# Performance work log

Hardware: AMD Instinct MI355X
Metric: run time of the kernel (lower is better)

Reference implementation:

```python
import jax, jax.numpy as jnp
import numpy as np

B, S, D, H = 1, 256, 128, 4
HD = D // H          # 32
EPS = 1e-5
SCALE = 1.0 / float(np.sqrt(HD))


def setup_inputs() -> dict:
    key = jax.random.key(0)
    ks = jax.random.split(key, 6)
    pair = jax.random.normal(ks[0], (B, S, S, D), dtype=jnp.float32)
    ln_w = jnp.ones((D,), dtype=jnp.float32)
    wq = jax.random.normal(ks[1], (D, D), dtype=jnp.float32) * 0.05
    wk = jax.random.normal(ks[2], (D, D), dtype=jnp.float32) * 0.05
    wv = jax.random.normal(ks[3], (D, D), dtype=jnp.float32) * 0.05
    wo = jax.random.normal(ks[4], (D, D), dtype=jnp.float32) * 0.05
    return {"pair": pair, "ln_w": ln_w, "wq": wq, "wk": wk, "wv": wv, "wo": wo}


def reference(pair, ln_w, wq, wk, wv, wo):
    b, s, _, d = pair.shape
    h, hd = H, HD
    # LayerNorm (weight only, no bias) over last dim
    mu = jnp.mean(pair, axis=-1, keepdims=True)
    var = jnp.mean((pair - mu) ** 2, axis=-1, keepdims=True)
    xn = (pair - mu) * jax.lax.rsqrt(var + EPS) * ln_w
    # starting=True: no transpose of the pair axes
    q = (xn @ wq.T).reshape(b, s, s, h, hd)
    k = (xn @ wk.T).reshape(b, s, s, h, hd)
    v = (xn @ wv.T).reshape(b, s, s, h, hd)
    # attention over the second seq axis (j), independent per row i
    scores = jnp.einsum("biqhd,bikhd->bihqk", q, k) * SCALE  # [b,i,h,q,k]
    p = jax.nn.softmax(scores, axis=-1)
    out = jnp.einsum("bihqk,bikhd->biqhd", p, v).reshape(b, s, s, d)
    return out @ wo.T
```

## Files before the change

### kernel.cpp

```cpp
#include <hip/hip_runtime.h>
#include <hip/hip_bf16.h>
#include <math.h>

#define S 256
#define D 128
#define H 4
#define HD 32
#define NT (S * S)

constexpr float EPS = 1e-5f;
constexpr float EXPC = 0.17677669529663687f * 1.44269504088896f;

typedef short bf16x8 __attribute__((ext_vector_type(8)));
typedef float floatx4 __attribute__((ext_vector_type(4)));

union BfBits { __hip_bfloat16 b; unsigned short u; };
__device__ inline unsigned short f2bf_bits(float f) {
  BfBits t;
  t.b = __float2bfloat16(f);
  return t.u;
}
__device__ inline short f2bf_s(float f) { return (short)f2bf_bits(f); }
__device__ inline float bfbits2f(unsigned short u) {
  union { float f; unsigned int i; } t;
  t.i = ((unsigned int)u) << 16;
  return t.f;
}
__device__ inline void split_bf(float x, unsigned short& hi, unsigned short& lo) {
  hi = f2bf_bits(x);
  lo = f2bf_bits(x - bfbits2f(hi));
}

__global__ __launch_bounds__(256) void wsplit_kernel(
    const float* __restrict__ wq, const float* __restrict__ wk,
    const float* __restrict__ wv, const float* __restrict__ wo,
    unsigned short* __restrict__ whi, unsigned short* __restrict__ wlo) {
  int idx = blockIdx.x * 256 + threadIdx.x;
  const float* srcs[4] = {wq, wk, wv, wo};
#pragma unroll
  for (int m = 0; m < 4; m++) {
    unsigned short hi, lo;
    split_bf(srcs[m][idx], hi, lo);
    whi[m * 16384 + idx] = hi;
    wlo[m * 16384 + idx] = lo;
  }
}

#define XPAD 8
__global__ __launch_bounds__(256, 4) void qkv_ln_mfma_kernel(
    const float* __restrict__ pair, const float* __restrict__ ln_w,
    const unsigned short* __restrict__ Whi,
    const unsigned short* __restrict__ Wlo, unsigned short* __restrict__ Qb,
    unsigned short* __restrict__ Kb, unsigned short* __restrict__ Vt) {
  __shared__ unsigned short xhi[64][D + XPAD];
  const int t0 = blockIdx.x * 64;
  const int wave = threadIdx.x >> 6;
  const int lane = threadIdx.x & 63;

  {
    float2 w2 = *(const float2*)(ln_w + lane * 2);
    for (int tt = 0; tt < 16; tt++) {
      int tok = wave * 16 + tt;
      float2 x = *(const float2*)(pair + (size_t)(t0 + tok) * D + lane * 2);
      float s = x.x + x.y;
#pragma unroll
      for (int o = 32; o > 0; o >>= 1) s += __shfl_xor(s, o);
      float mu = s * (1.0f / D);
      float a = x.x - mu;
      float b = x.y - mu;
      float vs = a * a + b * b;
#pragma unroll
      for (int o = 32; o > 0; o >>= 1) vs += __shfl_xor(vs, o);
      float r = rsqrtf(vs * (1.0f / D) + EPS);
      unsigned int h0 = f2bf_bits(a * r * w2.x);
      unsigned int h1 = f2bf_bits(b * r * w2.y);
      *(unsigned int*)&xhi[tok][lane * 2] = h0 | (h1 << 16);
    }
  }
  __syncthreads();

  const int c16 = lane & 15;
  const int quad = lane >> 4;
  const int i_ = t0 >> 8;
  const int jbase = t0 & 255;

  for (int mat = 0; mat < 3; mat++) {
    floatx4 acc[2][4];
#pragma unroll
    for (int mi = 0; mi < 2; mi++)
#pragma unroll
      for (int nt = 0; nt < 4; nt++) acc[mi][nt] = (floatx4){0.f, 0.f, 0.f, 0.f};

#pragma unroll 2
    for (int ks = 0; ks < 4; ks++) {
      const int k0 = ks * 32;
      bf16x8 bh[4];
#pragma unroll
      for (int nt = 0; nt < 4; nt++)
        bh[nt] = *(const bf16x8*)&xhi[nt * 16 + c16][k0 + quad * 8];
#pragma unroll
      for (int mi = 0; mi < 2; mi++) {
        const int m0 = (wave * 2 + mi) * 16;
        bf16x8 ah = *(const bf16x8*)(Whi + mat * 16384 + (m0 + c16) * D + k0 + quad * 8);
        bf16x8 al = *(const bf16x8*)(Wlo + mat * 16384 + (m0 + c16) * D + k0 + quad * 8);
#pragma unroll
        for (int nt = 0; nt < 4; nt++) {
          acc[mi][nt] = __builtin_amdgcn_mfma_f32_16x16x32_bf16(ah, bh[nt], acc[mi][nt], 0, 0, 0);
          acc[mi][nt] = __builtin_amdgcn_mfma_f32_16x16x32_bf16(al, bh[nt], acc[mi][nt], 0, 0, 0);
        }
      }
    }

#pragma unroll
    for (int mi = 0; mi < 2; mi++) {
      const int m0 = (wave * 2 + mi) * 16;
      const int d0 = m0 + quad * 4;
      const int h = d0 >> 5;
      const int hd = d0 & 31;
#pragma unroll
      for (int nt = 0; nt < 4; nt++) {
        const int j = jbase + nt * 16 + c16;
        floatx4 v4 = acc[mi][nt];
        if (mat < 2) {
          ushort4 pk;
          pk.x = f2bf_bits(v4[0]);
          pk.y = f2bf_bits(v4[1]);
          pk.z = f2bf_bits(v4[2]);
          pk.w = f2bf_bits(v4[3]);
          unsigned short* dst = (mat == 0) ? Qb : Kb;
          size_t off = (((size_t)h * S + i_) * S + j) * HD + hd;
          *(ushort4*)(dst + off) = pk;
        } else {
#pragma unroll
          for (int r = 0; r < 4; r++) {
            size_t off = (((size_t)h * S + i_) * HD + (hd + r)) * S + j;
            Vt[off] = f2bf_bits(v4[r]);
          }
        }
      }
    }
  }
}

#define OLD 133
__global__ __launch_bounds__(256, 4) void attn_oproj_kernel(
    const unsigned short* __restrict__ Qb, const unsigned short* __restrict__ Kb,
    const unsigned short* __restrict__ Vt, const unsigned short* __restrict__ Whi,
    const unsigned short* __restrict__ Wlo, float* __restrict__ out) {
  __shared__ unsigned int Ols[64][OLD];
  const int i = blockIdx.x;
  const int p = blockIdx.y;
  const int h = threadIdx.x >> 6;
  const int lane = threadIdx.x & 63;
  const int c = lane & 15;
  const int quad = lane >> 4;
  const int q0 = p * 64;

  const unsigned short* Qbase = Qb + (((size_t)h * S + i) * S) * HD;
  const unsigned short* Kbase = Kb + (((size_t)h * S + i) * S) * HD;
  const unsigned short* Vbase = Vt + (((size_t)h * S + i) * HD) * S;

  bf16x8 qf[4];
#pragma unroll
  for (int qt = 0; qt < 4; qt++)
    qf[qt] = *(const bf16x8*)(Qbase + (size_t)(q0 + qt * 16 + c) * HD + quad * 8);

  floatx4 acc[2][4];
#pragma unroll
  for (int dt = 0; dt < 2; dt++)
#pragma unroll
    for (int qt = 0; qt < 4; qt++) acc[dt][qt] = (floatx4){0.f, 0.f, 0.f, 0.f};
  float lsum[4] = {0.f, 0.f, 0.f, 0.f};

  const int permc = ((c >> 2) * 8) + (c & 3);

  for (int jb = 0; jb < S; jb += 32) {
    bf16x8 kf0 = *(const bf16x8*)(Kbase + (size_t)(jb + permc + 0) * HD + quad * 8);
    bf16x8 kf1 = *(const bf16x8*)(Kbase + (size_t)(jb + permc + 4) * HD + quad * 8);
    bf16x8 vf0 = *(const bf16x8*)(Vbase + (size_t)(0 * 16 + c) * S + jb + quad * 8);
    bf16x8 vf1 = *(const bf16x8*)(Vbase + (size_t)(1 * 16 + c) * S + jb + quad * 8);

#pragma unroll
    for (int qt = 0; qt < 4; qt++) {
      floatx4 s0 = __builtin_amdgcn_mfma_f32_16x16x32_bf16(
          kf0, qf[qt], (floatx4){0.f, 0.f, 0.f, 0.f}, 0, 0, 0);
      floatx4 s1 = __builtin_amdgcn_mfma_f32_16x16x32_bf16(
          kf1, qf[qt], (floatx4){0.f, 0.f, 0.f, 0.f}, 0, 0, 0);
      float pr[8];
#pragma unroll
      for (int r = 0; r < 4; r++) pr[r] = exp2f(s0[r] * EXPC);
#pragma unroll
      for (int r = 0; r < 4; r++) pr[4 + r] = exp2f(s1[r] * EXPC);
      float ls = 0.f;
#pragma unroll
      for (int r = 0; r < 8; r++) ls += pr[r];
      lsum[qt] += ls;
      bf16x8 pf;
#pragma unroll
      for (int r = 0; r < 8; r++) pf[r] = f2bf_s(pr[r]);
      acc[0][qt] = __builtin_amdgcn_mfma_f32_16x16x32_bf16(vf0, pf, acc[0][qt], 0, 0, 0);
      acc[1][qt] = __builtin_amdgcn_mfma_f32_16x16x32_bf16(vf1, pf, acc[1][qt], 0, 0, 0);
    }
  }

#pragma unroll
  for (int qt = 0; qt < 4; qt++) {
    float l = lsum[qt];
    l += __shfl_xor(l, 16);
    l += __shfl_xor(l, 32);
    lsum[qt] = 1.0f / l;
  }

#pragma unroll
  for (int t = 0; t < 4; t++) {
    const float inv = lsum[t];
#pragma unroll
    for (int dt = 0; dt < 2; dt++) {
      floatx4 v4 = acc[dt][t];
      uint4 st;
      unsigned short hh, ll;
      split_bf(v4[0] * inv, hh, ll); st.x = (unsigned)hh | ((unsigned)ll << 16);
      split_bf(v4[1] * inv, hh, ll); st.y = (unsigned)hh | ((unsigned)ll << 16);
      split_bf(v4[2] * inv, hh, ll); st.z = (unsigned)hh | ((unsigned)ll << 16);
      split_bf(v4[3] * inv, hh, ll); st.w = (unsigned)hh | ((unsigned)ll << 16);
      *(uint4*)&Ols[t * 16 + c][h * 32 + dt * 16 + quad * 4] = st;
    }
  }

  bf16x8 woh[2][4], wol[2][4];
#pragma unroll
  for (int mi = 0; mi < 2; mi++)
#pragma unroll
    for (int ks = 0; ks < 4; ks++) {
      const int m0 = h * 32 + mi * 16;
      woh[mi][ks] = *(const bf16x8*)(Whi + 3 * 16384 + (m0 + c) * D + ks * 32 + quad * 8);
      wol[mi][ks] = *(const bf16x8*)(Wlo + 3 * 16384 + (m0 + c) * D + ks * 32 + quad * 8);
    }

  __syncthreads();

  floatx4 oacc[2][4];
#pragma unroll
  for (int mi = 0; mi < 2; mi++)
#pragma unroll
    for (int nt = 0; nt < 4; nt++) oacc[mi][nt] = (floatx4){0.f, 0.f, 0.f, 0.f};

#pragma unroll
  for (int ks = 0; ks < 4; ks++) {
#pragma unroll
    for (int nt = 0; nt < 4; nt++) {
      const unsigned int* src = &Ols[nt * 16 + c][ks * 32 + quad * 8];
      uint4 u0 = *(const uint4*)(src);
      uint4 u1 = *(const uint4*)(src + 4);
      unsigned int bhw[4], blw[4];
      bhw[0] = (u0.x & 0xFFFFu) | (u0.y << 16);
      blw[0] = (u0.x >> 16) | (u0.y & 0xFFFF0000u);
      bhw[1] = (u0.z & 0xFFFFu) | (u0.w << 16);
      blw[1] = (u0.z >> 16) | (u0.w & 0xFFFF0000u);
      bhw[2] = (u1.x & 0xFFFFu) | (u1.y << 16);
      blw[2] = (u1.x >> 16) | (u1.y & 0xFFFF0000u);
      bhw[3] = (u1.z & 0xFFFFu) | (u1.w << 16);
      blw[3] = (u1.z >> 16) | (u1.w & 0xFFFF0000u);
      bf16x8 bh = *(bf16x8*)bhw;
      bf16x8 bl = *(bf16x8*)blw;
#pragma unroll
      for (int mi = 0; mi < 2; mi++) {
        oacc[mi][nt] = __builtin_amdgcn_mfma_f32_16x16x32_bf16(woh[mi][ks], bh, oacc[mi][nt], 0, 0, 0);
        oacc[mi][nt] = __builtin_amdgcn_mfma_f32_16x16x32_bf16(woh[mi][ks], bl, oacc[mi][nt], 0, 0, 0);
        oacc[mi][nt] = __builtin_amdgcn_mfma_f32_16x16x32_bf16(wol[mi][ks], bh, oacc[mi][nt], 0, 0, 0);
      }
    }
  }

#pragma unroll
  for (int mi = 0; mi < 2; mi++) {
    const int m0 = h * 32 + mi * 16;
#pragma unroll
    for (int nt = 0; nt < 4; nt++) {
      float4 st;
      st.x = oacc[mi][nt][0];
      st.y = oacc[mi][nt][1];
      st.z = oacc[mi][nt][2];
      st.w = oacc[mi][nt][3];
      *(float4*)(out + ((size_t)i * S + q0 + nt * 16 + c) * D + m0 + quad * 4) = st;
    }
  }
}

extern "C" void kernel_launch(void* const* d_in, const int* in_sizes, int n_in,
                              void* d_out, int out_size, void* d_ws,
                              size_t ws_size, hipStream_t stream) {
  const float* pair = (const float*)d_in[0];
  const float* ln_w = (const float*)d_in[1];
  const float* wq = (const float*)d_in[2];
  const float* wk = (const float*)d_in[3];
  const float* wv = (const float*)d_in[4];
  const float* wo = (const float*)d_in[5];
  float* out = (float*)d_out;

  const size_t NE = (size_t)NT * D;
  unsigned short* base = (unsigned short*)d_ws;
  unsigned short* Qb = base;
  unsigned short* Kb = base + NE;
  unsigned short* Vt = base + 2 * NE;
  unsigned short* Whi = base + 3 * NE;
  unsigned short* Wlo = base + 3 * NE + 4 * 16384;

  wsplit_kernel<<<64, 256, 0, stream>>>(wq, wk, wv, wo, Whi, Wlo);
  qkv_ln_mfma_kernel<<<NT / 64, 256, 0, stream>>>(pair, ln_w, Whi, Wlo, Qb, Kb,
                                                  Vt);
  attn_oproj_kernel<<<dim3(S, 4), 256, 0, stream>>>(Qb, Kb, Vt, Whi, Wlo, out);
}
```

Baseline: 163.6 us.

## Halve QKV block token tile, vectorize LayerNorm loads, swizzle LDS layout

The QKV projection kernel now handles 32 tokens per block instead of 64, so twice as many blocks launch and the occupancy hint goes from 4 to 8 blocks per CU. LayerNorm now reads 8 floats per lane with float4 loads, handles 4 tokens per wave at a time, and reduces over 16 lanes, replacing the previous per-token 64-lane loop. The padded LDS tile is replaced with an XOR-swizzled layout to avoid bank conflicts. In exchange, each block reuses every weight fragment fetched from global memory across half as many tokens, which doubles total weight reads.

```diff
diff --git a/kernel.cpp b/kernel.cpp
--- a/kernel.cpp
+++ b/kernel.cpp
@@ -46,65 +46,85 @@
   }
 }
 
-#define XPAD 8
-__global__ __launch_bounds__(256, 4) void qkv_ln_mfma_kernel(
+#define XS(row, col) ((col) ^ (((row) & 7) << 3))
+__global__ __launch_bounds__(256, 8) void qkv_ln_mfma_kernel(
     const float* __restrict__ pair, const float* __restrict__ ln_w,
     const unsigned short* __restrict__ Whi,
     const unsigned short* __restrict__ Wlo, unsigned short* __restrict__ Qb,
     unsigned short* __restrict__ Kb, unsigned short* __restrict__ Vt) {
-  __shared__ unsigned short xhi[64][D + XPAD];
-  const int t0 = blockIdx.x * 64;
+  __shared__ unsigned short xhi[32][D];
+  const int t0 = blockIdx.x * 32;
   const int wave = threadIdx.x >> 6;
   const int lane = threadIdx.x & 63;
-
-  {
-    float2 w2 = *(const float2*)(ln_w + lane * 2);
-    for (int tt = 0; tt < 16; tt++) {
-      int tok = wave * 16 + tt;
-      float2 x = *(const float2*)(pair + (size_t)(t0 + tok) * D + lane * 2);
-      float s = x.x + x.y;
-#pragma unroll
-      for (int o = 32; o > 0; o >>= 1) s += __shfl_xor(s, o);
-      float mu = s * (1.0f / D);
-      float a = x.x - mu;
-      float b = x.y - mu;
-      float vs = a * a + b * b;
-#pragma unroll
-      for (int o = 32; o > 0; o >>= 1) vs += __shfl_xor(vs, o);
-      float r = rsqrtf(vs * (1.0f / D) + EPS);
-      unsigned int h0 = f2bf_bits(a * r * w2.x);
-      unsigned int h1 = f2bf_bits(b * r * w2.y);
-      *(unsigned int*)&xhi[tok][lane * 2] = h0 | (h1 << 16);
-    }
-  }
-  __syncthreads();
-
   const int c16 = lane & 15;
   const int quad = lane >> 4;
+
+  {
+    float4 w0 = *(const float4*)(ln_w + c16 * 8);
+    float4 w1 = *(const float4*)(ln_w + c16 * 8 + 4);
+#pragma unroll
+    for (int g = 0; g < 2; g++) {
+      const int tok = wave * 8 + g * 4 + quad;
+      const float* src = pair + (size_t)(t0 + tok) * D + c16 * 8;
+      float4 x0 = *(const float4*)(src);
+      float4 x1 = *(const float4*)(src + 4);
+      float s = (x0.x + x0.y) + (x0.z + x0.w) + (x1.x + x1.y) + (x1.z + x1.w);
+      s += __shfl_xor(s, 1);
+      s += __shfl_xor(s, 2);
+      s += __shfl_xor(s, 4);
+      s += __shfl_xor(s, 8);
+      const float mu = s * (1.0f / D);
+      float a[8];
+      a[0] = x0.x - mu; a[1] = x0.y - mu; a[2] = x0.z - mu; a[3] = x0.w - mu;
+      a[4] = x1.x - mu; a[5] = x1.y - mu; a[6] = x1.z - mu; a[7] = x1.w - mu;
+      float vs = 0.f;
+#pragma unroll
+      for (int r = 0; r < 8; r++) vs = fmaf(a[r], a[r], vs);
+      vs += __shfl_xor(vs, 1);
+      vs += __shfl_xor(vs, 2);
+      vs += __shfl_xor(vs, 4);
+      vs += __shfl_xor(vs, 8);
+      const float rinv = rsqrtf(vs * (1.0f / D) + EPS);
+      const float w[8] = {w0.x, w0.y, w0.z, w0.w, w1.x, w1.y, w1.z, w1.w};
+      unsigned int u[4];
+#pragma unroll
+      for (int r = 0; r < 4; r++) {
+        unsigned int h0 = f2bf_bits(a[2 * r] * rinv * w[2 * r]);
+        unsigned int h1 = f2bf_bits(a[2 * r + 1] * rinv * w[2 * r + 1]);
+        u[r] = h0 | (h1 << 16);
+      }
+      uint4 st = {u[0], u[1], u[2], u[3]};
+      *(uint4*)&xhi[tok][XS(tok, c16 * 8)] = st;
+    }
+  }
+  __syncthreads();
+
   const int i_ = t0 >> 8;
   const int jbase = t0 & 255;
 
   for (int mat = 0; mat < 3; mat++) {
-    floatx4 acc[2][4];
+    floatx4 acc[2][2];
 #pragma unroll
     for (int mi = 0; mi < 2; mi++)
 #pragma unroll
-      for (int nt = 0; nt < 4; nt++) acc[mi][nt] = (floatx4){0.f, 0.f, 0.f, 0.f};
+      for (int nt = 0; nt < 2; nt++) acc[mi][nt] = (floatx4){0.f, 0.f, 0.f, 0.f};
 
 #pragma unroll 2
     for (int ks = 0; ks < 4; ks++) {
       const int k0 = ks * 32;
-      bf16x8 bh[4];
-#pragma unroll
-      for (int nt = 0; nt < 4; nt++)
-        bh[nt] = *(const bf16x8*)&xhi[nt * 16 + c16][k0 + quad * 8];
+      bf16x8 bh[2];
+#pragma unroll
+      for (int nt = 0; nt < 2; nt++) {
+        const int row = nt * 16 + c16;
+        bh[nt] = *(const bf16x8*)&xhi[row][XS(row, k0 + quad * 8)];
+      }
 #pragma unroll
       for (int mi = 0; mi < 2; mi++) {
         const int m0 = (wave * 2 + mi) * 16;
         bf16x8 ah = *(const bf16x8*)(Whi + mat * 16384 + (m0 + c16) * D + k0 + quad * 8);
         bf16x8 al = *(const bf16x8*)(Wlo + mat * 16384 + (m0 + c16) * D + k0 + quad * 8);
 #pragma unroll
-        for (int nt = 0; nt < 4; nt++) {
+        for (int nt = 0; nt < 2; nt++) {
           acc[mi][nt] = __builtin_amdgcn_mfma_f32_16x16x32_bf16(ah, bh[nt], acc[mi][nt], 0, 0, 0);
           acc[mi][nt] = __builtin_amdgcn_mfma_f32_16x16x32_bf16(al, bh[nt], acc[mi][nt], 0, 0, 0);
         }
@@ -118,7 +138,7 @@
       const int h = d0 >> 5;
       const int hd = d0 & 31;
 #pragma unroll
-      for (int nt = 0; nt < 4; nt++) {
+      for (int nt = 0; nt < 2; nt++) {
         const int j = jbase + nt * 16 + c16;
         floatx4 v4 = acc[mi][nt];
         if (mat < 2) {
@@ -307,7 +327,7 @@
   unsigned short* Wlo = base + 3 * NE + 4 * 16384;
 
   wsplit_kernel<<<64, 256, 0, stream>>>(wq, wk, wv, wo, Whi, Wlo);
-  qkv_ln_mfma_kernel<<<NT / 64, 256, 0, stream>>>(pair, ln_w, Whi, Wlo, Qb, Kb,
+  qkv_ln_mfma_kernel<<<NT / 32, 256, 0, stream>>>(pair, ln_w, Whi, Wlo, Qb, Kb,
                                                   Vt);
   attn_oproj_kernel<<<dim3(S, 4), 256, 0, stream>>>(Qb, Kb, Vt, Whi, Wlo, out);
 }
```

New measurement: 171.5 us. 4.8% more time.
